# Optimization experiments

Measured on AMD Instinct MI355X. Metric: run time of the kernel, lower is better.

## Reference

```python
import jax, jax.numpy as jnp
import numpy as np

N_NODES = 50000
N_EDGES = 640000
IN_DIM = 128
HID = 128
OUT_DIM = 16
BATCH = 2
EPS = 1e-5


def setup_inputs() -> dict:
    key = jax.random.key(0)
    ks = jax.random.split(key, 12)
    x = jax.random.normal(ks[0], (BATCH, N_NODES, IN_DIM), dtype=jnp.float32)
    edge_index = jax.random.randint(ks[1], (2, N_EDGES), 0, N_NODES, dtype=jnp.int32)
    # learned per-edge log-weights (initialized ~0 like nn.Parameter(zeros), small noise for a nontrivial test)
    edge_weight_param = 0.01 * jax.random.normal(ks[2], (N_EDGES,), dtype=jnp.float32)
    s1 = 1.0 / np.sqrt(IN_DIM)
    s2 = 1.0 / np.sqrt(HID)
    W1 = jax.random.uniform(ks[3], (IN_DIM, HID), minval=-s1, maxval=s1, dtype=jnp.float32)
    b1 = jnp.zeros((HID,), jnp.float32)
    W2 = jax.random.uniform(ks[4], (HID, HID), minval=-s2, maxval=s2, dtype=jnp.float32)
    b2 = jnp.zeros((HID,), jnp.float32)
    g1 = jnp.ones((HID,), jnp.float32); be1 = jnp.zeros((HID,), jnp.float32)
    g2 = jnp.ones((HID,), jnp.float32); be2 = jnp.zeros((HID,), jnp.float32)
    Wc = jax.random.uniform(ks[5], (HID, OUT_DIM), minval=-s2, maxval=s2, dtype=jnp.float32)
    bc = jax.random.uniform(ks[6], (OUT_DIM,), minval=-s2, maxval=s2, dtype=jnp.float32)
    return {"x": x, "edge_index": edge_index, "edge_weight_param": edge_weight_param,
            "W1": W1, "b1": b1, "W2": W2, "b2": b2,
            "g1": g1, "be1": be1, "g2": g2, "be2": be2,
            "Wc": Wc, "bc": bc}


def _gcn_norm(edge_index, edge_weight):
    # PyG GCNConv: add self-loops (weight 1), symmetric D^-1/2 A D^-1/2 normalization
    row = jnp.concatenate([edge_index[0], jnp.arange(N_NODES, dtype=edge_index.dtype)])
    col = jnp.concatenate([edge_index[1], jnp.arange(N_NODES, dtype=edge_index.dtype)])
    ew = jnp.concatenate([edge_weight, jnp.ones((N_NODES,), edge_weight.dtype)])
    deg = jax.ops.segment_sum(ew, col, num_segments=N_NODES)
    dinv = jnp.where(deg > 0, jax.lax.rsqrt(jnp.maximum(deg, 1e-30)), 0.0)
    norm = dinv[row] * ew * dinv[col]
    return row, col, norm


def _gcn_conv(x, W, b, row, col, norm):
    # x: [B, N, F_in] -> [B, N, F_out]; gather-scale-scatter over edges
    xw = x @ W                                   # [B, N, H]
    msg = xw[:, row, :] * norm[None, :, None]    # [B, E+N, H]
    out = jax.vmap(lambda m: jax.ops.segment_sum(m, col, num_segments=N_NODES))(msg)
    return out + b


def _batchnorm(h, gamma, beta):
    # training-mode BN over flattened (B*N) rows, biased variance, eps=1e-5
    B, N, F = h.shape
    hf = h.reshape(-1, F)
    mu = hf.mean(axis=0)
    var = hf.var(axis=0)
    return (((hf - mu) * jax.lax.rsqrt(var + EPS)) * gamma + beta).reshape(B, N, F)


def reference(x, edge_index, edge_weight_param, W1, b1, W2, b2, g1, be1, g2, be2, Wc, bc):
    edge_weight = jnp.exp(edge_weight_param)  # learned exp edge weights
    row, col, norm = _gcn_norm(edge_index, edge_weight)
    h = jax.nn.relu(_gcn_conv(x, W1, b1, row, col, norm))
    h = _batchnorm(h, g1, be1)
    # dropout is identity in eval / deterministic reference
    h = jax.nn.relu(_gcn_conv(h, W2, b2, row, col, norm))
    h = _batchnorm(h, g2, be2)
    return h @ Wc + bc  # [B, N, OUT_DIM]
```

## Files before the change

kernel.cpp:

```cpp
#include <hip/hip_runtime.h>
#include <hip/hip_bf16.h>
#include <cstdint>
#include <cstddef>

#define N_NODES 50000
#define N_EDGES 640000
#define ROWS    100000
#define HID     128
#define OUTD    16
#define AGG_BLOCKS 2048
#define MID_BLOCKS 32
#define SCAN_BLOCKS 196
#define GEMM_BLOCKS 512
#define G2_BLOCKS   800
#define GEMM_TILES  (ROWS / 16)
#define PAIR_TILES  (N_NODES / 16)
#define EG_BLOCKS   3500
#define EG_GEMM_WAVES 4000

typedef __attribute__((ext_vector_type(8))) uint16_t ushort8;
typedef __attribute__((ext_vector_type(8))) __bf16   bf16x8;
typedef __attribute__((ext_vector_type(4))) float    floatx4;

union FragU { ushort8 u; bf16x8 b; };

__device__ __forceinline__ float bf_lo(uint32_t u){
  union { uint32_t u; float f; } c; c.u = u << 16; return c.f;
}
__device__ __forceinline__ float bf_hi(uint32_t u){
  union { uint32_t u; float f; } c; c.u = u & 0xffff0000u; return c.f;
}
__device__ __forceinline__ uint16_t f2bf(float f){
  union { float f; uint32_t u; } c; c.f = f;
  uint32_t u = c.u;
  uint32_t r = (u + 0x7fffu + ((u >> 16) & 1u)) >> 16;
  return (uint16_t)r;
}

__device__ __forceinline__ void pack_w(int t, const float* __restrict__ W,
                                       const float* sca ,
                                       uint16_t* __restrict__ WP){
  int L = t & 63;
  int s = (t >> 6) & 3;
  int c = t >> 8;
  int n = (c >> 1) * 32 + 2 * (L & 15) + (c & 1);
  int k0 = s * 32 + (L >> 4) * 8;
  ushort8 r;
#pragma unroll
  for (int j = 0; j < 8; j++){
    float w = W[(size_t)(k0 + j) * HID + n];
    if (sca) w *= sca[k0 + j];
    r[j] = f2bf(w);
  }
  *((ushort8*)(WP + (size_t)t * 8)) = r;
}

__global__ void k_initpack(unsigned long long* __restrict__ dc,
                           const float* __restrict__ W1, uint16_t* __restrict__ WP1,
                           unsigned int* __restrict__ cursor){
  int b = blockIdx.x;
  if (b < SCAN_BLOCKS){
    int i = b * 256 + threadIdx.x;
    if (i < N_NODES) dc[i] = 0ull;
  } else {
    if (b == SCAN_BLOCKS && threadIdx.x == 0) *cursor = 0u;
    pack_w((b - SCAN_BLOCKS) * 256 + threadIdx.x, W1, nullptr, WP1);
  }
}

__global__ __launch_bounds__(256, 2) void k_edge_gemm1(const int* __restrict__ ei,
                                                       const float* __restrict__ ewp,
                                                       unsigned long long* __restrict__ dc,
                                                       unsigned int* __restrict__ slot,
                                                       const float* __restrict__ X,
                                                       const uint16_t* __restrict__ WP,
                                                       uint16_t* __restrict__ Y){
  const int b = blockIdx.x;
  const int g = b % 7;
  if (g < 5){
    const int eb = (b / 7) * 5 + g;
    const int e = eb * 256 + threadIdx.x;
    float w = expf(ewp[e]);
    int c = ei[N_EDGES + e];
    unsigned long long inc = (1ull << 44) | (unsigned long long)(w * 1048576.0f + 0.5f);
    unsigned long long old = atomicAdd(&dc[c], inc);
    slot[e] = (unsigned int)(old >> 44);
    return;
  }
  const int lane = threadIdx.x & 63;
  const int wid  = threadIdx.x >> 6;
  const int gw   = ((b / 7) * 2 + (g - 5)) * 4 + wid;
  const int m    = lane & 15;
  const int kq   = lane >> 4;

  FragU wf[8][4];
#pragma unroll
  for (int c = 0; c < 8; c++)
#pragma unroll
    for (int s = 0; s < 4; s++)
      wf[c][s].u = *((const ushort8*)(WP + (size_t)(((c * 4 + s) * 64 + lane) * 8)));

  unsigned long long* Yq = (unsigned long long*)Y;
  for (int t = gw; t < PAIR_TILES; t += EG_GEMM_WAVES){
    const int nb = t * 16;
    uint32_t pr0[16];
    {
      FragU af[4];
#pragma unroll
      for (int s = 0; s < 4; s++){
        const float* p = X + (size_t)(nb + m) * HID + s * 32 + kq * 8;
        floatx4 f0 = *((const floatx4*)p);
        floatx4 f1 = *((const floatx4*)(p + 4));
        ushort8 r;
#pragma unroll
        for (int j = 0; j < 4; j++){ r[j] = f2bf(f0[j]); r[j + 4] = f2bf(f1[j]); }
        af[s].u = r;
      }
      floatx4 acc[8];
#pragma unroll
      for (int c = 0; c < 8; c++) acc[c] = floatx4{0.f, 0.f, 0.f, 0.f};
#pragma unroll
      for (int s = 0; s < 4; s++)
#pragma unroll
        for (int c = 0; c < 8; c++)
          acc[c] = __builtin_amdgcn_mfma_f32_16x16x32_bf16(af[s].b, wf[c][s].b, acc[c], 0, 0, 0);
#pragma unroll
      for (int t4 = 0; t4 < 4; t4++)
#pragma unroll
        for (int i = 0; i < 4; i++)
          pr0[t4 * 4 + i] = (uint32_t)f2bf(acc[2 * t4][i]) | ((uint32_t)f2bf(acc[2 * t4 + 1][i]) << 16);
    }
    {
      FragU af[4];
#pragma unroll
      for (int s = 0; s < 4; s++){
        const float* p = X + (size_t)(N_NODES + nb + m) * HID + s * 32 + kq * 8;
        floatx4 f0 = *((const floatx4*)p);
        floatx4 f1 = *((const floatx4*)(p + 4));
        ushort8 r;
#pragma unroll
        for (int j = 0; j < 4; j++){ r[j] = f2bf(f0[j]); r[j + 4] = f2bf(f1[j]); }
        af[s].u = r;
      }
      floatx4 acc[8];
#pragma unroll
      for (int c = 0; c < 8; c++) acc[c] = floatx4{0.f, 0.f, 0.f, 0.f};
#pragma unroll
      for (int s = 0; s < 4; s++)
#pragma unroll
        for (int c = 0; c < 8; c++)
          acc[c] = __builtin_amdgcn_mfma_f32_16x16x32_bf16(af[s].b, wf[c][s].b, acc[c], 0, 0, 0);
#pragma unroll
      for (int t4 = 0; t4 < 4; t4++)
#pragma unroll
        for (int i = 0; i < 4; i++){
          uint32_t pr1 = (uint32_t)f2bf(acc[2 * t4][i]) | ((uint32_t)f2bf(acc[2 * t4 + 1][i]) << 16);
          Yq[(size_t)(nb + kq * 4 + i) * 64 + t4 * 16 + m] =
              (unsigned long long)pr0[t4 * 4 + i] | ((unsigned long long)pr1 << 32);
        }
    }
  }
}

__global__ void k_alloc(const unsigned long long* __restrict__ dc,
                        unsigned long long* __restrict__ rp2,
                        float* __restrict__ dinv,
                        unsigned int* __restrict__ cursor){
  __shared__ int sd[256];
  __shared__ unsigned int sbase;
  const int tid = threadIdx.x;
  const int i = blockIdx.x * 256 + tid;
  int cnt = 0;
  if (i < N_NODES){
    unsigned long long v = dc[i];
    cnt = (int)(v >> 44);
    float deg = 1.0f + (float)((double)(v & ((1ull << 44) - 1)) * (1.0 / 1048576.0));
    dinv[i] = 1.0f / sqrtf(deg);
  }
  sd[tid] = cnt;
  __syncthreads();
  for (int off = 1; off < 256; off <<= 1){
    int t = (tid >= off) ? sd[tid - off] : 0;
    __syncthreads();
    sd[tid] += t;
    __syncthreads();
  }
  if (tid == 255) sbase = atomicAdd(cursor, (unsigned int)sd[255]);
  __syncthreads();
  if (i < N_NODES){
    unsigned int start = sbase + (unsigned int)(sd[tid] - cnt);
    rp2[i] = ((unsigned long long)(unsigned int)cnt << 32) | start;
  }
}

__global__ void k_fill(const int* __restrict__ ei, const float* __restrict__ ewp,
                       const float* __restrict__ dinv, const unsigned int* __restrict__ slot,
                       const unsigned long long* __restrict__ rp2,
                       unsigned long long* __restrict__ edg){
  int e = blockIdx.x * 256 + threadIdx.x;
  if (e < N_EDGES){
    int r = ei[e];
    int c = ei[N_EDGES + e];
    float w = expf(ewp[e]);
    float nrm = dinv[r] * w * dinv[c];
    int p = (int)(unsigned int)rp2[c] + (int)slot[e];
    edg[p] = ((unsigned long long)__float_as_uint(nrm) << 32) | (unsigned int)r;
  }
}

__global__ __launch_bounds__(256, 2) void k_gemm2(const uint16_t* __restrict__ X,
                                                  const uint16_t* __restrict__ WP,
                                                  uint16_t* __restrict__ Y){
  const int lane = threadIdx.x & 63;
  const int wid  = threadIdx.x >> 6;
  const int gw   = blockIdx.x * 4 + wid;
  const int nw   = G2_BLOCKS * 4;
  const int m    = lane & 15;
  const int kq   = lane >> 4;

  FragU wf[8][4];
#pragma unroll
  for (int c = 0; c < 8; c++)
#pragma unroll
    for (int s = 0; s < 4; s++)
      wf[c][s].u = *((const ushort8*)(WP + (size_t)(((c * 4 + s) * 64 + lane) * 8)));

  unsigned long long* Yq = (unsigned long long*)Y;
  for (int t = gw; t < PAIR_TILES; t += nw){
    const int nb = t * 16;
    uint32_t pr0[16];
    {
      FragU af[4];
#pragma unroll
      for (int s = 0; s < 4; s++)
        af[s].u = *((const ushort8*)(X + (size_t)(nb + m) * HID + s * 32 + kq * 8));
      floatx4 acc[8];
#pragma unroll
      for (int c = 0; c < 8; c++) acc[c] = floatx4{0.f, 0.f, 0.f, 0.f};
#pragma unroll
      for (int s = 0; s < 4; s++)
#pragma unroll
        for (int c = 0; c < 8; c++)
          acc[c] = __builtin_amdgcn_mfma_f32_16x16x32_bf16(af[s].b, wf[c][s].b, acc[c], 0, 0, 0);
#pragma unroll
      for (int t4 = 0; t4 < 4; t4++)
#pragma unroll
        for (int i = 0; i < 4; i++)
          pr0[t4 * 4 + i] = (uint32_t)f2bf(acc[2 * t4][i]) | ((uint32_t)f2bf(acc[2 * t4 + 1][i]) << 16);
    }
    {
      FragU af[4];
#pragma unroll
      for (int s = 0; s < 4; s++)
        af[s].u = *((const ushort8*)(X + (size_t)(N_NODES + nb + m) * HID + s * 32 + kq * 8));
      floatx4 acc[8];
#pragma unroll
      for (int c = 0; c < 8; c++) acc[c] = floatx4{0.f, 0.f, 0.f, 0.f};
#pragma unroll
      for (int s = 0; s < 4; s++)
#pragma unroll
        for (int c = 0; c < 8; c++)
          acc[c] = __builtin_amdgcn_mfma_f32_16x16x32_bf16(af[s].b, wf[c][s].b, acc[c], 0, 0, 0);
#pragma unroll
      for (int t4 = 0; t4 < 4; t4++)
#pragma unroll
        for (int i = 0; i < 4; i++){
          uint32_t pr1 = (uint32_t)f2bf(acc[2 * t4][i]) | ((uint32_t)f2bf(acc[2 * t4 + 1][i]) << 16);
          Yq[(size_t)(nb + kq * 4 + i) * 64 + t4 * 16 + m] =
              (unsigned long long)pr0[t4 * 4 + i] | ((unsigned long long)pr1 << 32);
        }
    }
  }
}

__global__ __launch_bounds__(256) void k_cls_mfma(const uint16_t* __restrict__ H,
                                                  const uint16_t* __restrict__ WPC,
                                                  const float* __restrict__ cvec,
                                                  float* __restrict__ out){
  const int lane = threadIdx.x & 63;
  const int wid  = threadIdx.x >> 6;
  const int gw   = blockIdx.x * 4 + wid;
  const int nw   = GEMM_BLOCKS * 4;
  const int m    = lane & 15;
  const int kq   = lane >> 4;

  FragU wf[4];
#pragma unroll
  for (int s = 0; s < 4; s++)
    wf[s].u = *((const ushort8*)(WPC + (size_t)((s * 64 + lane) * 8)));
  const float cv = cvec[m];

  for (int t = gw; t < GEMM_TILES; t += nw){
    const int row0 = t * 16;
    FragU af[4];
#pragma unroll
    for (int s = 0; s < 4; s++)
      af[s].u = *((const ushort8*)(H + (size_t)(row0 + m) * HID + s * 32 + kq * 8));
    floatx4 acc = floatx4{0.f, 0.f, 0.f, 0.f};
#pragma unroll
    for (int s = 0; s < 4; s++)
      acc = __builtin_amdgcn_mfma_f32_16x16x32_bf16(af[s].b, wf[s].b, acc, 0, 0, 0);
#pragma unroll
    for (int i = 0; i < 4; i++)
      out[(size_t)(row0 + kq * 4 + i) * OUTD + m] = acc[i] + cv;
  }
}

__global__ __launch_bounds__(256) void k_agg(const uint16_t* __restrict__ XW,
                                             const unsigned long long* __restrict__ rp2,
                                             const unsigned long long* __restrict__ edg,
                                             const float* __restrict__ dinv,
                                             const float* __restrict__ bias,
                                             const float* __restrict__ cvec,
                                             uint16_t* __restrict__ H,
                                             float* __restrict__ psum,
                                             float* __restrict__ pssq){
  __shared__ float lsum[128];
  __shared__ float lssq[128];
  const int tid = threadIdx.x;
  if (tid < 128){ lsum[tid] = 0.f; lssq[tid] = 0.f; }
  __syncthreads();

  const int lane = tid & 63;
  const int wid  = tid >> 6;
  const int gw   = blockIdx.x * 4 + wid;
  const int nw   = AGG_BLOCKS * 4;
  const unsigned long long* Xq = (const unsigned long long*)XW;
  uint32_t* Hu = (uint32_t*)H;
  const int f0 = lane * 2;
  const float b0 = bias[f0], b1 = bias[f0 + 1];
  const float c0 = cvec ? cvec[f0] : 0.f;
  const float c1 = cvec ? cvec[f0 + 1] : 0.f;
  float ts0 = 0.f, ts1 = 0.f, tq0 = 0.f, tq1 = 0.f;
  const int lu = lane & 7;

  int node = gw;
  if (node < N_NODES){
    unsigned long long rc = rp2[node];
    int e0 = (int)(unsigned int)rc, e1 = e0 + (int)(rc >> 32);
    float di = dinv[node];
    unsigned long long sv = Xq[(size_t)node * 64 + lane];
    unsigned long long rec = 0ull;
    if (e0 < e1){
      int a = e0 + lu; if (a > N_EDGES - 1) a = N_EDGES - 1;
      rec = edg[a];
    }
    while (true){
      const int nn = node + nw;
      const bool more = (nn < N_NODES);
      int ne0 = 0, ne1 = 0; float ndi = 0.f; unsigned long long nsv = 0ull;
      if (more){
        unsigned long long nrc = rp2[nn];
        ne0 = (int)(unsigned int)nrc; ne1 = ne0 + (int)(nrc >> 32);
        ndi = dinv[nn];
        nsv = Xq[(size_t)nn * 64 + lane];
      }

      const float sn = di * di;
      const uint32_t s0 = (uint32_t)sv, s1 = (uint32_t)(sv >> 32);
      float a0x = sn * bf_lo(s0), a0y = sn * bf_hi(s0);
      float a1x = sn * bf_lo(s1), a1y = sn * bf_hi(s1);
      float wsum = sn;

      for (int e = e0; e < e1; e += 8){
        const int r = e1 - e;
        const uint32_t rlo = (uint32_t)rec;
        const uint32_t rhi = (uint32_t)(rec >> 32);
        const int pe = (r > 8) ? (e + 8) : (more ? ne0 : -1);
        if (pe >= 0){
          int a = pe + lu; if (a > N_EDGES - 1) a = N_EDGES - 1;
          rec = edg[a];
        }
        unsigned long long q[8];
        if (r >= 8){
#pragma unroll
          for (int u = 0; u < 8; u++)
            q[u] = Xq[(size_t)(uint32_t)__builtin_amdgcn_readlane((int)rlo, u) * 64 + lane];
#pragma unroll
          for (int u = 0; u < 8; u++){
            const float w = __uint_as_float((uint32_t)__builtin_amdgcn_readlane((int)rhi, u));
            const uint32_t g0 = (uint32_t)q[u], g1 = (uint32_t)(q[u] >> 32);
            a0x = fmaf(w, bf_lo(g0), a0x); a0y = fmaf(w, bf_hi(g0), a0y);
            a1x = fmaf(w, bf_lo(g1), a1x); a1y = fmaf(w, bf_hi(g1), a1y);
            wsum += w;
          }
        } else {
#pragma unroll
          for (int u = 0; u < 8; u++)
            if (u < r)
              q[u] = Xq[(size_t)(uint32_t)__builtin_amdgcn_readlane((int)rlo, u) * 64 + lane];
#pragma unroll
          for (int u = 0; u < 8; u++)
            if (u < r){
              const float w = __uint_as_float((uint32_t)__builtin_amdgcn_readlane((int)rhi, u));
              const uint32_t g0 = (uint32_t)q[u], g1 = (uint32_t)(q[u] >> 32);
              a0x = fmaf(w, bf_lo(g0), a0x); a0y = fmaf(w, bf_hi(g0), a0y);
              a1x = fmaf(w, bf_lo(g1), a1x); a1y = fmaf(w, bf_hi(g1), a1y);
              wsum += w;
            }
        }
      }
      if (e0 == e1 && more){
        int a = ne0 + lu; if (a > N_EDGES - 1) a = N_EDGES - 1;
        rec = edg[a];
      }

      a0x = fmaxf(fmaf(wsum, c0, a0x) + b0, 0.f); a0y = fmaxf(fmaf(wsum, c1, a0y) + b1, 0.f);
      a1x = fmaxf(fmaf(wsum, c0, a1x) + b0, 0.f); a1y = fmaxf(fmaf(wsum, c1, a1y) + b1, 0.f);
      Hu[(size_t)node * 64 + lane]             = (uint32_t)f2bf(a0x) | ((uint32_t)f2bf(a0y) << 16);
      Hu[(size_t)(N_NODES + node) * 64 + lane] = (uint32_t)f2bf(a1x) | ((uint32_t)f2bf(a1y) << 16);
      ts0 += a0x + a1x; ts1 += a0y + a1y;
      tq0 += a0x * a0x + a1x * a1x; tq1 += a0y * a0y + a1y * a1y;

      if (!more) break;
      node = nn; e0 = ne0; e1 = ne1; di = ndi; sv = nsv;
    }
  }

  atomicAdd(&lsum[f0],     ts0); atomicAdd(&lsum[f0 + 1], ts1);
  atomicAdd(&lssq[f0],     tq0); atomicAdd(&lssq[f0 + 1], tq1);
  __syncthreads();
  if (tid < 128){
    psum[(size_t)blockIdx.x * 128 + tid] = lsum[tid];
    pssq[(size_t)blockIdx.x * 128 + tid] = lssq[tid];
  }
}

__global__ __launch_bounds__(256) void k_bnmid(const float* __restrict__ psum,
                                               const float* __restrict__ pssq,
                                               float* __restrict__ msum,
                                               float* __restrict__ mssq){
  __shared__ float ss[2][128];
  __shared__ float sq[2][128];
  const int tid = threadIdx.x;
  const int f  = tid & 127;
  const int sl = tid >> 7;
  const int rows_per = AGG_BLOCKS / MID_BLOCKS;
  const int base = blockIdx.x * rows_per;
  float s = 0.f, q = 0.f;
  for (int r = base + sl; r < base + rows_per; r += 2){
    s += psum[(size_t)r * 128 + f];
    q += pssq[(size_t)r * 128 + f];
  }
  ss[sl][f] = s; sq[sl][f] = q;
  __syncthreads();
  if (tid < 128){
    msum[(size_t)blockIdx.x * 128 + tid] = ss[0][tid] + ss[1][tid];
    mssq[(size_t)blockIdx.x * 128 + tid] = sq[0][tid] + sq[1][tid];
  }
}

__device__ __forceinline__ void bn_finalize_lds(const float* __restrict__ msum,
                                                const float* __restrict__ mssq,
                                                const float* __restrict__ gamma,
                                                const float* __restrict__ beta,
                                                float* ssc, float* ssh){
  const int tid = threadIdx.x;
  if (tid < 128){
    float S = 0.f, Q = 0.f;
#pragma unroll
    for (int b = 0; b < MID_BLOCKS; b++){
      S += msum[(size_t)b * 128 + tid];
      Q += mssq[(size_t)b * 128 + tid];
    }
    const float inv = 1.0f / (float)ROWS;
    float mu = S * inv;
    float var = fmaxf(Q * inv - mu * mu, 0.f);
    float rstd = 1.0f / sqrtf(var + 1e-5f);
    float sc = gamma[tid] * rstd;
    ssc[tid] = sc;
    ssh[tid] = fmaf(-mu, sc, beta[tid]);
  }
  __syncthreads();
}

__global__ void k_prep2(const float* __restrict__ msum, const float* __restrict__ mssq,
                        const float* __restrict__ gamma, const float* __restrict__ beta,
                        const float* __restrict__ W2,
                        uint16_t* __restrict__ WP2, float* __restrict__ C2){
  __shared__ float ssc[128];
  __shared__ float ssh[128];
  bn_finalize_lds(msum, mssq, gamma, beta, ssc, ssh);
  if (blockIdx.x < 8){
    pack_w(blockIdx.x * 256 + threadIdx.x, W2, ssc, WP2);
  } else if (threadIdx.x < 128){
    const int j = threadIdx.x;
    float a = 0.f;
    for (int k = 0; k < HID; k++) a = fmaf(ssh[k], W2[(size_t)k * HID + j], a);
    C2[j] = a;
  }
}

__global__ void k_prepc(const float* __restrict__ msum, const float* __restrict__ mssq,
                        const float* __restrict__ gamma, const float* __restrict__ beta,
                        const float* __restrict__ Wc, const float* __restrict__ bc,
                        uint16_t* __restrict__ WPC, float* __restrict__ CVC){
  __shared__ float ssc[128];
  __shared__ float ssh[128];
  bn_finalize_lds(msum, mssq, gamma, beta, ssc, ssh);
  if (blockIdx.x == 0){
    int t = threadIdx.x;
    int L = t & 63;
    int s = t >> 6;
    int n = L & 15;
    int k0 = s * 32 + (L >> 4) * 8;
    ushort8 r;
#pragma unroll
    for (int j = 0; j < 8; j++)
      r[j] = f2bf(ssc[k0 + j] * Wc[(size_t)(k0 + j) * OUTD + n]);
    *((ushort8*)(WPC + (size_t)t * 8)) = r;
  } else if (threadIdx.x < OUTD){
    const int j = threadIdx.x;
    float a = bc[j];
    for (int k = 0; k < HID; k++) a = fmaf(ssh[k], Wc[(size_t)k * OUTD + j], a);
    CVC[j] = a;
  }
}

extern "C" void kernel_launch(void* const* d_in, const int* in_sizes, int n_in,
                              void* d_out, int out_size, void* d_ws, size_t ws_size,
                              hipStream_t stream){
  const float* x   = (const float*)d_in[0];
  const int*   ei  = (const int*)d_in[1];
  const float* ewp = (const float*)d_in[2];
  const float* W1  = (const float*)d_in[3];
  const float* b1  = (const float*)d_in[4];
  const float* W2  = (const float*)d_in[5];
  const float* b2  = (const float*)d_in[6];
  const float* g1  = (const float*)d_in[7];
  const float* be1 = (const float*)d_in[8];
  const float* g2  = (const float*)d_in[9];
  const float* be2 = (const float*)d_in[10];
  const float* Wc  = (const float*)d_in[11];
  const float* bc  = (const float*)d_in[12];
  float* out = (float*)d_out;

  char* wsb = (char*)d_ws;
  size_t off = 0;
  auto give = [&](size_t bytes) -> void* {
    void* p = wsb + off;
    off = (off + bytes + 255) & ~(size_t)255;
    return p;
  };
  uint16_t* XW  = (uint16_t*)give((size_t)ROWS * 128 * 2);
  uint16_t* Hb  = (uint16_t*)give((size_t)ROWS * 128 * 2);
  unsigned long long* DC  = (unsigned long long*)give((size_t)N_NODES * 8);
  unsigned long long* EDG = (unsigned long long*)give((size_t)N_EDGES * 8);
  unsigned int* SLOT = (unsigned int*)give((size_t)N_EDGES * 4);
  float* DINV   = (float*)give((size_t)N_NODES * 4);
  unsigned long long* RP2 = (unsigned long long*)give((size_t)N_NODES * 8);
  unsigned int* CURSOR = (unsigned int*)give(256);
  float* PSUM   = (float*)give((size_t)AGG_BLOCKS * 128 * 4);
  float* PSSQ   = (float*)give((size_t)AGG_BLOCKS * 128 * 4);
  float* MSUM   = (float*)give((size_t)MID_BLOCKS * 128 * 4);
  float* MSSQ   = (float*)give((size_t)MID_BLOCKS * 128 * 4);
  uint16_t* WP1 = (uint16_t*)give((size_t)HID * HID * 2);
  uint16_t* WP2 = (uint16_t*)give((size_t)HID * HID * 2);
  uint16_t* WPC = (uint16_t*)give((size_t)HID * OUTD * 2);
  float* C2     = (float*)give(512);
  float* CVC    = (float*)give(64);
  (void)ws_size; (void)n_in; (void)in_sizes; (void)out_size;

  k_initpack<<<SCAN_BLOCKS + 8, 256, 0, stream>>>(DC, W1, WP1, CURSOR);
  k_edge_gemm1<<<EG_BLOCKS, 256, 0, stream>>>(ei, ewp, DC, SLOT, x, WP1, XW);
  k_alloc<<<SCAN_BLOCKS, 256, 0, stream>>>(DC, RP2, DINV, CURSOR);
  k_fill<<<(N_EDGES + 255) / 256, 256, 0, stream>>>(ei, ewp, DINV, SLOT, RP2, EDG);
  k_agg<<<AGG_BLOCKS, 256, 0, stream>>>(XW, RP2, EDG, DINV, b1, nullptr, Hb, PSUM, PSSQ);
  k_bnmid<<<MID_BLOCKS, 256, 0, stream>>>(PSUM, PSSQ, MSUM, MSSQ);
  k_prep2<<<9, 256, 0, stream>>>(MSUM, MSSQ, g1, be1, W2, WP2, C2);
  k_gemm2<<<G2_BLOCKS, 256, 0, stream>>>(Hb, WP2, XW);
  k_agg<<<AGG_BLOCKS, 256, 0, stream>>>(XW, RP2, EDG, DINV, b2, C2, Hb, PSUM, PSSQ);
  k_bnmid<<<MID_BLOCKS, 256, 0, stream>>>(PSUM, PSSQ, MSUM, MSSQ);
  k_prepc<<<2, 256, 0, stream>>>(MSUM, MSSQ, g2, be2, Wc, bc, WPC, CVC);
  k_cls_mfma<<<GEMM_BLOCKS, 256, 0, stream>>>(Hb, WPC, CVC, out);
}
```

Before: 315.2 us.

## Split aggregation work per node into two feature halves across waves

The sparse aggregation kernel now assigns each wave one half of the 128-column interleaved row (node, half) instead of a whole node, doubling the work items to 2*N_NODES. Each lane gathers 4 bytes per edge instead of 8, and writes outputs into the batch-split H layout using lane parity for the batch. The aim is more parallelism and shorter per-wave latency chains. In exchange, edge records and row pointers are read twice, gathers become narrower, and the block-level stats accumulation has more branches.

```diff
diff --git a/kernel.cpp b/kernel.cpp
--- a/kernel.cpp
+++ b/kernel.cpp
@@ -325,41 +325,48 @@
   const int wid  = tid >> 6;
   const int gw   = blockIdx.x * 4 + wid;
   const int nw   = AGG_BLOCKS * 4;
-  const unsigned long long* Xq = (const unsigned long long*)XW;
+  const uint32_t* Xu = (const uint32_t*)XW;
   uint32_t* Hu = (uint32_t*)H;
-  const int f0 = lane * 2;
-  const float b0 = bias[f0], b1 = bias[f0 + 1];
-  const float c0 = cvec ? cvec[f0] : 0.f;
-  const float c1 = cvec ? cvec[f0 + 1] : 0.f;
-  float ts0 = 0.f, ts1 = 0.f, tq0 = 0.f, tq1 = 0.f;
+  const int bb = lane & 1;
+  const int pl = lane >> 1;
   const int lu = lane & 7;
-
-  int node = gw;
-  if (node < N_NODES){
+  float ts00 = 0.f, ts01 = 0.f, tq00 = 0.f, tq01 = 0.f;
+  float ts10 = 0.f, ts11 = 0.f, tq10 = 0.f, tq11 = 0.f;
+
+  int wrk = gw;
+  if (wrk < 2 * N_NODES){
+    int fh   = (wrk >= N_NODES) ? 1 : 0;
+    int node = wrk - fh * N_NODES;
     unsigned long long rc = rp2[node];
     int e0 = (int)(unsigned int)rc, e1 = e0 + (int)(rc >> 32);
     float di = dinv[node];
-    unsigned long long sv = Xq[(size_t)node * 64 + lane];
+    uint32_t sv = Xu[(size_t)node * 128 + fh * 64 + lane];
     unsigned long long rec = 0ull;
     if (e0 < e1){
       int a = e0 + lu; if (a > N_EDGES - 1) a = N_EDGES - 1;
       rec = edg[a];
     }
     while (true){
-      const int nn = node + nw;
-      const bool more = (nn < N_NODES);
-      int ne0 = 0, ne1 = 0; float ndi = 0.f; unsigned long long nsv = 0ull;
+      const int nwrk = wrk + nw;
+      const bool more = (nwrk < 2 * N_NODES);
+      int nfh = 0, nnode = 0, ne0 = 0, ne1 = 0; float ndi = 0.f; uint32_t nsv = 0u;
       if (more){
-        unsigned long long nrc = rp2[nn];
+        nfh   = (nwrk >= N_NODES) ? 1 : 0;
+        nnode = nwrk - nfh * N_NODES;
+        unsigned long long nrc = rp2[nnode];
         ne0 = (int)(unsigned int)nrc; ne1 = ne0 + (int)(nrc >> 32);
-        ndi = dinv[nn];
-        nsv = Xq[(size_t)nn * 64 + lane];
+        ndi = dinv[nnode];
+        nsv = Xu[(size_t)nnode * 128 + nfh * 64 + lane];
       }
 
+      const int f0 = fh * 64 + (lane & 62);
+      const float b0 = bias[f0], b1 = bias[f0 + 1];
+      const float c0 = cvec ? cvec[f0] : 0.f;
+      const float c1 = cvec ? cvec[f0 + 1] : 0.f;
+      const size_t xoff = (size_t)(fh * 64 + lane);
+
       const float sn = di * di;
-      const uint32_t s0 = (uint32_t)sv, s1 = (uint32_t)(sv >> 32);
-      float a0x = sn * bf_lo(s0), a0y = sn * bf_hi(s0);
-      float a1x = sn * bf_lo(s1), a1y = sn * bf_hi(s1);
+      float a0 = sn * bf_lo(sv), a1 = sn * bf_hi(sv);
       float wsum = sn;
 
       for (int e = e0; e < e1; e += 8){
@@ -371,31 +378,27 @@
           int a = pe + lu; if (a > N_EDGES - 1) a = N_EDGES - 1;
           rec = edg[a];
         }
-        unsigned long long q[8];
+        uint32_t q[8];
         if (r >= 8){
 #pragma unroll
           for (int u = 0; u < 8; u++)
-            q[u] = Xq[(size_t)(uint32_t)__builtin_amdgcn_readlane((int)rlo, u) * 64 + lane];
+            q[u] = Xu[(size_t)(uint32_t)__builtin_amdgcn_readlane((int)rlo, u) * 128 + xoff];
 #pragma unroll
           for (int u = 0; u < 8; u++){
             const float w = __uint_as_float((uint32_t)__builtin_amdgcn_readlane((int)rhi, u));
-            const uint32_t g0 = (uint32_t)q[u], g1 = (uint32_t)(q[u] >> 32);
-            a0x = fmaf(w, bf_lo(g0), a0x); a0y = fmaf(w, bf_hi(g0), a0y);
-            a1x = fmaf(w, bf_lo(g1), a1x); a1y = fmaf(w, bf_hi(g1), a1y);
+            a0 = fmaf(w, bf_lo(q[u]), a0); a1 = fmaf(w, bf_hi(q[u]), a1);
             wsum += w;
           }
         } else {
 #pragma unroll
           for (int u = 0; u < 8; u++)
             if (u < r)
-              q[u] = Xq[(size_t)(uint32_t)__builtin_amdgcn_readlane((int)rlo, u) * 64 + lane];
+              q[u] = Xu[(size_t)(uint32_t)__builtin_amdgcn_readlane((int)rlo, u) * 128 + xoff];
 #pragma unroll
           for (int u = 0; u < 8; u++)
             if (u < r){
               const float w = __uint_as_float((uint32_t)__builtin_amdgcn_readlane((int)rhi, u));
-              const uint32_t g0 = (uint32_t)q[u], g1 = (uint32_t)(q[u] >> 32);
-              a0x = fmaf(w, bf_lo(g0), a0x); a0y = fmaf(w, bf_hi(g0), a0y);
-              a1x = fmaf(w, bf_lo(g1), a1x); a1y = fmaf(w, bf_hi(g1), a1y);
+              a0 = fmaf(w, bf_lo(q[u]), a0); a1 = fmaf(w, bf_hi(q[u]), a1);
               wsum += w;
             }
         }
@@ -405,20 +408,23 @@
         rec = edg[a];
       }
 
-      a0x = fmaxf(fmaf(wsum, c0, a0x) + b0, 0.f); a0y = fmaxf(fmaf(wsum, c1, a0y) + b1, 0.f);
-      a1x = fmaxf(fmaf(wsum, c0, a1x) + b0, 0.f); a1y = fmaxf(fmaf(wsum, c1, a1y) + b1, 0.f);
-      Hu[(size_t)node * 64 + lane]             = (uint32_t)f2bf(a0x) | ((uint32_t)f2bf(a0y) << 16);
-      Hu[(size_t)(N_NODES + node) * 64 + lane] = (uint32_t)f2bf(a1x) | ((uint32_t)f2bf(a1y) << 16);
-      ts0 += a0x + a1x; ts1 += a0y + a1y;
-      tq0 += a0x * a0x + a1x * a1x; tq1 += a0y * a0y + a1y * a1y;
+      a0 = fmaxf(fmaf(wsum, c0, a0) + b0, 0.f);
+      a1 = fmaxf(fmaf(wsum, c1, a1) + b1, 0.f);
+      Hu[(size_t)(bb * N_NODES + node) * 64 + fh * 32 + pl] =
+          (uint32_t)f2bf(a0) | ((uint32_t)f2bf(a1) << 16);
+      if (fh == 0){ ts00 += a0; ts01 += a1; tq00 += a0 * a0; tq01 += a1 * a1; }
+      else        { ts10 += a0; ts11 += a1; tq10 += a0 * a0; tq11 += a1 * a1; }
 
       if (!more) break;
-      node = nn; e0 = ne0; e1 = ne1; di = ndi; sv = nsv;
-    }
-  }
-
-  atomicAdd(&lsum[f0],     ts0); atomicAdd(&lsum[f0 + 1], ts1);
-  atomicAdd(&lssq[f0],     tq0); atomicAdd(&lssq[f0 + 1], tq1);
+      wrk = nwrk; fh = nfh; node = nnode; e0 = ne0; e1 = ne1; di = ndi; sv = nsv;
+    }
+  }
+
+  const int fe = lane & 62;
+  atomicAdd(&lsum[fe],          ts00); atomicAdd(&lsum[fe + 1],      ts01);
+  atomicAdd(&lsum[64 + fe],     ts10); atomicAdd(&lsum[64 + fe + 1], ts11);
+  atomicAdd(&lssq[fe],          tq00); atomicAdd(&lssq[fe + 1],      tq01);
+  atomicAdd(&lssq[64 + fe],     tq10); atomicAdd(&lssq[64 + fe + 1], tq11);
   __syncthreads();
   if (tid < 128){
     psum[(size_t)blockIdx.x * 128 + tid] = lsum[tid];
```

Result: slower. 334.1 us (+6.0%).
